# Optimization experiments

Hardware: AMD Instinct MI355X
Metric: run time of the kernel (lower is better)

The kernel has to match this reference:

```python
import jax, jax.numpy as jnp
import numpy as np

B, S, HID = 1, 2048, 2048
NH, NKV, D = 32, 8, 64
GROUPS = NH // NKV
THETA = 10000.0


def _rope_tables(seq_len, dim):
    inv_freq = 1.0 / (THETA ** (jnp.arange(0, dim, 2, dtype=jnp.float32) / dim))
    t = jnp.arange(seq_len, dtype=jnp.float32)
    freqs = jnp.outer(t, inv_freq)            # [S, D/2]
    emb = jnp.concatenate([freqs, freqs], axis=-1)  # [S, D]
    return jnp.cos(emb), jnp.sin(emb)


def _rotate_half(x):
    x1, x2 = jnp.split(x, 2, axis=-1)
    return jnp.concatenate([-x2, x1], axis=-1)


def setup_inputs() -> dict:
    key = jax.random.key(0)
    ks = jax.random.split(key, 8)
    hidden_states = jax.random.normal(ks[0], (B, S, HID), dtype=jnp.float32)
    # additive causal mask, 0 on/below diagonal, -1e9 above
    causal = jnp.tril(jnp.ones((S, S), dtype=bool))
    attention_mask = jnp.where(causal, 0.0, -1e9).astype(jnp.float32)[None, None]
    sc = 0.02
    Wq = sc * jax.random.normal(ks[1], (NH * D, HID), dtype=jnp.float32)
    bq = jnp.zeros((NH * D,), dtype=jnp.float32)
    Wk = sc * jax.random.normal(ks[2], (NKV * D, HID), dtype=jnp.float32)
    bk = jnp.zeros((NKV * D,), dtype=jnp.float32)
    Wv = sc * jax.random.normal(ks[3], (NKV * D, HID), dtype=jnp.float32)
    bv = jnp.zeros((NKV * D,), dtype=jnp.float32)
    Wo = sc * jax.random.normal(ks[4], (HID, NH * D), dtype=jnp.float32)
    return {"hidden_states": hidden_states, "attention_mask": attention_mask,
            "Wq": Wq, "bq": bq, "Wk": Wk, "bk": bk, "Wv": Wv, "bv": bv, "Wo": Wo}


def reference(hidden_states, attention_mask, Wq, bq, Wk, bk, Wv, bv, Wo):
    b, s, _ = hidden_states.shape
    q = (hidden_states @ Wq.T + bq).reshape(b, s, NH, D).transpose(0, 2, 1, 3)   # [B,NH,S,D]
    k = (hidden_states @ Wk.T + bk).reshape(b, s, NKV, D).transpose(0, 2, 1, 3)  # [B,NKV,S,D]
    v = (hidden_states @ Wv.T + bv).reshape(b, s, NKV, D).transpose(0, 2, 1, 3)
    cos, sin = _rope_tables(s, D)
    cos = cos[None, None]; sin = sin[None, None]
    q = q * cos + _rotate_half(q) * sin
    k = k * cos + _rotate_half(k) * sin
    # GQA: repeat KV heads to match query heads
    k = jnp.repeat(k, GROUPS, axis=1)  # [B,NH,S,D]
    v = jnp.repeat(v, GROUPS, axis=1)
    scores = jnp.einsum('bhqd,bhkd->bhqk', q, k) / jnp.sqrt(jnp.float32(D))
    scores = jnp.clip(scores, -50.0, 50.0)
    scores = scores + attention_mask
    probs = jax.nn.softmax(scores.astype(jnp.float32), axis=-1).astype(q.dtype)
    attn = jnp.einsum('bhqk,bhkd->bhqd', probs, v)
    attn = attn.transpose(0, 2, 1, 3).reshape(b, s, NH * D)
    return attn @ Wo.T
```

## Files before the change

kernel.cpp:

```cpp
#include <hip/hip_runtime.h>
#include <hip/hip_bf16.h>
#include <stdint.h>

typedef unsigned short u16;
typedef unsigned int u32;

#define S_LEN 2048
#define HID 2048
#define NH 32
#define NKV 8
#define HD 64
#define PIT 2080

using f32x4 = __attribute__((ext_vector_type(4))) float;
using bfrag = __attribute__((ext_vector_type(8))) short;

__device__ __forceinline__ float b2f(u16 u) {
  union { u32 i; float f; } c; c.i = ((u32)u) << 16; return c.f;
}
__device__ __forceinline__ u16 f2b(float f) {
  union { float f; u32 i; } c; c.f = f;
  u32 r = c.i + 0x7fffu + ((c.i >> 16) & 1u);
  return (u16)(r >> 16);
}
__device__ __forceinline__ uint4 cvt8(const float* __restrict__ p) {
  float4 a = *(const float4*)p;
  float4 b = *(const float4*)(p + 4);
  uint4 r;
  r.x = (u32)f2b(a.x) | ((u32)f2b(a.y) << 16);
  r.y = (u32)f2b(a.z) | ((u32)f2b(a.w) << 16);
  r.z = (u32)f2b(b.x) | ((u32)f2b(b.y) << 16);
  r.w = (u32)f2b(b.z) | ((u32)f2b(b.w) << 16);
  return r;
}

__device__ __forceinline__ void gl2lds16(const u16* g, u16* l) {
  __builtin_amdgcn_global_load_lds(
      (const __attribute__((address_space(1))) void*)g,
      (__attribute__((address_space(3))) void*)l,
      16, 0, 0);
}

#define WAITBAR(N) asm volatile("s_waitcnt vmcnt(" #N ")\ns_barrier" ::: "memory")

__global__ void conv_all(const float* __restrict__ hid, const float* __restrict__ Wq,
                         const float* __restrict__ Wk, const float* __restrict__ Wv,
                         u16* __restrict__ hidb, u16* __restrict__ Wqkvb) {
  int row = blockIdx.x;
  int col = threadIdx.x * 8;
  const float* src; u16* dst;
  if (row < 2048)      { src = hid + (size_t)row * 2048;          dst = hidb  + (size_t)row * PIT; }
  else if (row < 4096) { src = Wq + (size_t)(row - 2048) * 2048;  dst = Wqkvb + (size_t)(row - 2048) * PIT; }
  else if (row < 4608) { src = Wk + (size_t)(row - 4096) * 2048;  dst = Wqkvb + (size_t)(row - 4096 + 2048) * PIT; }
  else                 { src = Wv + (size_t)(row - 4608) * 2048;  dst = Wqkvb + (size_t)(row - 4608 + 2560) * PIT; }
  *(uint4*)(dst + col) = cvt8(src + col);
}

__global__ void conv_all_w(const float* __restrict__ hid, const float* __restrict__ Wq,
                           const float* __restrict__ Wk, const float* __restrict__ Wv,
                           const float* __restrict__ Wo,
                           u16* __restrict__ hidb, u16* __restrict__ Wqkvb,
                           u16* __restrict__ Wob) {
  int row = blockIdx.x;
  int col = threadIdx.x * 8;
  const float* src; u16* dst;
  if (row < 2048)      { src = hid + (size_t)row * 2048;          dst = hidb  + (size_t)row * PIT; }
  else if (row < 4096) { src = Wq + (size_t)(row - 2048) * 2048;  dst = Wqkvb + (size_t)(row - 2048) * PIT; }
  else if (row < 4608) { src = Wk + (size_t)(row - 4096) * 2048;  dst = Wqkvb + (size_t)(row - 4096 + 2048) * PIT; }
  else if (row < 5120) { src = Wv + (size_t)(row - 4608) * 2048;  dst = Wqkvb + (size_t)(row - 4608 + 2560) * PIT; }
  else                 { src = Wo + (size_t)(row - 5120) * 2048;  dst = Wob   + (size_t)(row - 5120) * PIT; }
  *(uint4*)(dst + col) = cvt8(src + col);
}

__global__ void conv_f2b_p(const float* __restrict__ in, u16* __restrict__ out, int n8) {
  int i = blockIdx.x * 256 + threadIdx.x;
  if (i >= n8) return;
  int row = i >> 8;
  int col = (i & 255) * 8;
  *(uint4*)(out + (size_t)row * PIT + col) = cvt8(in + (size_t)row * 2048 + col);
}

__global__ __launch_bounds__(256, 3) void gemm_qkv(
    const u16* __restrict__ A, const u16* __restrict__ B,
    const float* __restrict__ bq, const float* __restrict__ bk, const float* __restrict__ bv,
    u16* __restrict__ Qb, u16* __restrict__ Kb, u16* __restrict__ Vt)
{
  __shared__ __align__(16) u16 As[2 * 4096];
  __shared__ __align__(16) u16 Bs[2 * 8192];

  const int tid  = threadIdx.x;
  const int m0   = blockIdx.y * 64;
  const int n0   = blockIdx.x * 128;
  const int lane = tid & 63;
  const int w    = tid >> 6;
  const int wm   = w >> 1, wn = w & 1;
  const int quad = lane >> 4, l16 = lane & 15;

  const int sr = tid >> 3;
  const int sg = (tid & 7) ^ (sr & 7);
  const u16* gA = A + (size_t)(m0 + sr) * PIT + sg * 8;
  const u16* gB = B + (size_t)(n0 + sr) * PIT + sg * 8;

#define STAGE_G(bi, k0)                                                          \
  do {                                                                           \
    gl2lds16(gA + (k0),                    As + (bi) * 4096 + tid * 8);          \
    gl2lds16(gA + (size_t)32 * PIT + (k0), As + (bi) * 4096 + 2048 + tid * 8);   \
    gl2lds16(gB + (k0),                    Bs + (bi) * 8192 + tid * 8);          \
    gl2lds16(gB + (size_t)32 * PIT + (k0), Bs + (bi) * 8192 + 2048 + tid * 8);   \
    gl2lds16(gB + (size_t)64 * PIT + (k0), Bs + (bi) * 8192 + 4096 + tid * 8);   \
    gl2lds16(gB + (size_t)96 * PIT + (k0), Bs + (bi) * 8192 + 6144 + tid * 8);   \
  } while (0)

  f32x4 zero = {0.f, 0.f, 0.f, 0.f};
  f32x4 acc[2][4];
#pragma unroll
  for (int mi = 0; mi < 2; ++mi)
#pragma unroll
    for (int ni = 0; ni < 4; ++ni) acc[mi][ni] = zero;

  STAGE_G(0, 0);

  int cur = 0;
  for (int k = 0; k < 32; ++k) {
    WAITBAR(0);
    if (k + 1 < 32) STAGE_G(cur ^ 1, (k + 1) * 64);
    const u16* as = As + cur * 4096;
    const u16* bs = Bs + cur * 8192;

#pragma unroll
    for (int kk = 0; kk < 2; ++kk) {
      const int sA = ((kk * 4 + quad) ^ (l16 & 7)) * 8;
      bfrag af[2], bf[4];
#pragma unroll
      for (int i = 0; i < 2; ++i)
        af[i] = *(const bfrag*)&as[(wm * 32 + i * 16 + l16) * 64 + sA];
#pragma unroll
      for (int i = 0; i < 4; ++i)
        bf[i] = *(const bfrag*)&bs[(wn * 64 + i * 16 + l16) * 64 + sA];
#pragma unroll
      for (int mi = 0; mi < 2; ++mi)
#pragma unroll
        for (int ni = 0; ni < 4; ++ni)
          acc[mi][ni] = __builtin_amdgcn_mfma_f32_16x16x32_bf16(af[mi], bf[ni], acc[mi][ni], 0, 0, 0);
    }
    cur ^= 1;
  }
#undef STAGE_G

  __syncthreads();
  u16* strip = As + w * 1152;
  const int rr = lane >> 2;
  const int co = (lane & 3) * 8;

  if (n0 < 2048) {
#pragma unroll
    for (int mi = 0; mi < 2; ++mi) {
#pragma unroll
      for (int n01 = 0; n01 < 2; ++n01)
#pragma unroll
        for (int i = 0; i < 4; ++i) {
          int d  = n01 * 16 + l16;
          int c1 = n0 + wn * 64 + d;
          float x1 = acc[mi][n01][i]     + bq[c1];
          float x2 = acc[mi][n01 + 2][i] + bq[c1 + 32];
          float inv = exp2f(-(float)d * 0.41524101186092034f);
          float ang = (float)(m0 + wm * 32 + mi * 16 + quad * 4 + i) * inv;
          float cs = cosf(ang), sn = sinf(ang);
          strip[(quad * 4 + i) * 72 + d]      = f2b(x1 * cs - x2 * sn);
          strip[(quad * 4 + i) * 72 + d + 32] = f2b(x2 * cs + x1 * sn);
        }
      uint4 v0 = *(const uint4*)&strip[rr * 72 + co];
      uint4 v1 = *(const uint4*)&strip[rr * 72 + 32 + co];
      size_t gb2 = (size_t)(m0 + wm * 32 + mi * 16 + rr) * 2048 + n0 + wn * 64;
      *(uint4*)(Qb + gb2 + co)      = v0;
      *(uint4*)(Qb + gb2 + 32 + co) = v1;
    }
  } else if (n0 < 2560) {
    int cb = (n0 - 2048) + wn * 64;
#pragma unroll
    for (int mi = 0; mi < 2; ++mi) {
#pragma unroll
      for (int n01 = 0; n01 < 2; ++n01)
#pragma unroll
        for (int i = 0; i < 4; ++i) {
          int d  = n01 * 16 + l16;
          int cg = cb + d;
          float x1 = acc[mi][n01][i]     + bk[cg];
          float x2 = acc[mi][n01 + 2][i] + bk[cg + 32];
          float inv = exp2f(-(float)d * 0.41524101186092034f);
          float ang = (float)(m0 + wm * 32 + mi * 16 + quad * 4 + i) * inv;
          float cs = cosf(ang), sn = sinf(ang);
          strip[(quad * 4 + i) * 72 + d]      = f2b(x1 * cs - x2 * sn);
          strip[(quad * 4 + i) * 72 + d + 32] = f2b(x2 * cs + x1 * sn);
        }
      uint4 v0 = *(const uint4*)&strip[rr * 72 + co];
      uint4 v1 = *(const uint4*)&strip[rr * 72 + 32 + co];
      size_t gb2 = (size_t)(m0 + wm * 32 + mi * 16 + rr) * 512 + cb;
      *(uint4*)(Kb + gb2 + co)      = v0;
      *(uint4*)(Kb + gb2 + 32 + co) = v1;
    }
  } else {
    int cgb = (n0 - 2560) + wn * 64;
#pragma unroll
    for (int ni = 0; ni < 4; ++ni) {
      float bvv = bv[cgb + ni * 16 + l16];
#pragma unroll
      for (int mi = 0; mi < 2; ++mi)
#pragma unroll
        for (int i = 0; i < 4; ++i)
          strip[l16 * 72 + mi * 16 + quad * 4 + i] = f2b(acc[mi][ni][i] + bvv);
      uint4 v0 = *(const uint4*)&strip[rr * 72 + co];
      size_t gb2 = (size_t)(cgb + ni * 16 + rr) * PIT + m0 + wm * 32;
      *(uint4*)(Vt + gb2 + co) = v0;
    }
  }
}

__global__ __launch_bounds__(256, 3) void gemm_o(
    const u16* __restrict__ A, const u16* __restrict__ B, float* __restrict__ C)
{
  __shared__ __align__(16) u16 As[2 * 4096];
  __shared__ __align__(16) u16 Bs[2 * 8192];

  const int tid  = threadIdx.x;
  const int m0   = blockIdx.y * 64;
  const int n0   = blockIdx.x * 128;
  const int lane = tid & 63;
  const int w    = tid >> 6;
  const int wm   = w >> 1, wn = w & 1;
  const int quad = lane >> 4, l16 = lane & 15;

  const int sr = tid >> 3;
  const int sg = (tid & 7) ^ (sr & 7);
  const u16* gA = A + (size_t)(m0 + sr) * PIT + sg * 8;
  const u16* gB = B + (size_t)(n0 + sr) * PIT + sg * 8;

#define STAGE_O(bi, k0)                                                          \
  do {                                                                           \
    gl2lds16(gA + (k0),                    As + (bi) * 4096 + tid * 8);          \
    gl2lds16(gA + (size_t)32 * PIT + (k0), As + (bi) * 4096 + 2048 + tid * 8);   \
    gl2lds16(gB + (k0),                    Bs + (bi) * 8192 + tid * 8);          \
    gl2lds16(gB + (size_t)32 * PIT + (k0), Bs + (bi) * 8192 + 2048 + tid * 8);   \
    gl2lds16(gB + (size_t)64 * PIT + (k0), Bs + (bi) * 8192 + 4096 + tid * 8);   \
    gl2lds16(gB + (size_t)96 * PIT + (k0), Bs + (bi) * 8192 + 6144 + tid * 8);   \
  } while (0)

  f32x4 zero = {0.f, 0.f, 0.f, 0.f};
  f32x4 acc[2][4];
#pragma unroll
  for (int mi = 0; mi < 2; ++mi)
#pragma unroll
    for (int ni = 0; ni < 4; ++ni) acc[mi][ni] = zero;

  STAGE_O(0, 0);

  int cur = 0;
  for (int k = 0; k < 32; ++k) {
    WAITBAR(0);
    if (k + 1 < 32) STAGE_O(cur ^ 1, (k + 1) * 64);
    const u16* as = As + cur * 4096;
    const u16* bs = Bs + cur * 8192;

#pragma unroll
    for (int kk = 0; kk < 2; ++kk) {
      const int sA = ((kk * 4 + quad) ^ (l16 & 7)) * 8;
      bfrag af[2], bf[4];
#pragma unroll
      for (int i = 0; i < 2; ++i)
        af[i] = *(const bfrag*)&as[(wm * 32 + i * 16 + l16) * 64 + sA];
#pragma unroll
      for (int i = 0; i < 4; ++i)
        bf[i] = *(const bfrag*)&bs[(wn * 64 + i * 16 + l16) * 64 + sA];
#pragma unroll
      for (int mi = 0; mi < 2; ++mi)
#pragma unroll
        for (int ni = 0; ni < 4; ++ni)
          acc[mi][ni] = __builtin_amdgcn_mfma_f32_16x16x32_bf16(af[mi], bf[ni], acc[mi][ni], 0, 0, 0);
    }
    cur ^= 1;
  }
#undef STAGE_O

#pragma unroll
  for (int ni = 0; ni < 4; ++ni) {
    int col = n0 + wn * 64 + ni * 16 + l16;
#pragma unroll
    for (int mi = 0; mi < 2; ++mi)
#pragma unroll
      for (int i = 0; i < 4; ++i) {
        int row = m0 + wm * 32 + mi * 16 + quad * 4 + i;
        C[(size_t)row * 2048 + col] = acc[mi][ni][i];
      }
  }
}

#define SM_SC 0.18033688011112042f

__global__ __launch_bounds__(256, 2) void attn_flash7(
    const u16* __restrict__ Qb, const u16* __restrict__ Kb,
    const u16* __restrict__ Vt, u16* __restrict__ Ab)
{
  __shared__ __align__(16) u16 Ks[2][2][64 * 64];
  __shared__ __align__(16) u16 Vs[2][2][64 * 64];
  __shared__ __align__(16) u16 Ps[4][16][72];

  const int h    = blockIdx.x;
  const int p    = blockIdx.y;
  const int kvh  = h >> 2;
  const int tid  = threadIdx.x;
  const int lane = tid & 63;
  const int w    = tid >> 6;
  const int quad = lane >> 4, l16 = lane & 15;

  const int qtA = 31 - p, qtB = p;
  const int nA  = qtA + 1;

  const int c0  = w * 128 + lane;
  const int r0  = c0 >> 3,        s0 = c0 & 7;
  const int r1  = (c0 + 64) >> 3, s1 = (c0 + 64) & 7;
  const int sg0 = s0 ^ (r0 & 7);
  const int sg1 = s1 ^ (r1 & 7);
  const u16* Ksrc0 = Kb + (size_t)r0 * 512 + kvh * 64 + sg0 * 8;
  const u16* Ksrc1 = Kb + (size_t)r1 * 512 + kvh * 64 + sg1 * 8;
  const u16* Vsrc0 = Vt + (size_t)(kvh * 64 + r0) * PIT + sg0 * 8;
  const u16* Vsrc1 = Vt + (size_t)(kvh * 64 + r1) * PIT + sg1 * 8;

#define KBOF(t) ((t) < nA ? (t) : (t) - nA)

#define STAGEKV(buf, half, kb)                                                  \
  do {                                                                          \
    gl2lds16(Ksrc0 + (size_t)(kb) * 32768, &Ks[buf][half][0] + c0 * 8);         \
    gl2lds16(Ksrc1 + (size_t)(kb) * 32768, &Ks[buf][half][0] + (c0 + 64) * 8);  \
    gl2lds16(Vsrc0 + (kb) * 64,            &Vs[buf][half][0] + c0 * 8);         \
    gl2lds16(Vsrc1 + (kb) * 64,            &Vs[buf][half][0] + (c0 + 64) * 8);  \
  } while (0)

  STAGEKV(0, 0, 0);
  STAGEKV(0, 1, 1);

  bfrag qfA0, qfA1, qfB0, qfB1;
  {
    const u16* qa = Qb + (size_t)(qtA * 64 + w * 16 + l16) * 2048 + h * 64 + quad * 8;
    const u16* qb = Qb + (size_t)(qtB * 64 + w * 16 + l16) * 2048 + h * 64 + quad * 8;
    qfA0 = *(const bfrag*)qa;  qfA1 = *(const bfrag*)(qa + 32);
    qfB0 = *(const bfrag*)qb;  qfB1 = *(const bfrag*)(qb + 32);
  }
  bfrag q0 = qfA0, q1 = qfA1;

  f32x4 zero = {0.f, 0.f, 0.f, 0.f};
  f32x4 o_acc[4];
  float lpart[4];
#pragma unroll
  for (int nb = 0; nb < 4; ++nb) { o_acc[nb] = zero; lpart[nb] = 0.f; }

  const int swz = (l16 & 7) * 8;
  int qt = qtA;
  int cur = 0;

  for (int T = 0; T < 17; ++T) {
    WAITBAR(0);
    if (T < 16) {
      STAGEKV(cur ^ 1, 0, KBOF(2 * T + 2));
      STAGEKV(cur ^ 1, 1, KBOF(2 * T + 3));
    }

    for (int hh = 0; hh < 2; ++hh) {
      const int t = 2 * T + hh;
      if (t >= 33) break;
      if (t == nA) { q0 = qfB0; q1 = qfB1; qt = qtB; }

      const u16* ks = &Ks[cur][hh][0];
      const u16* vs = &Vs[cur][hh][0];

      bfrag kf0[4], kf1[4];
#pragma unroll
      for (int nb = 0; nb < 4; ++nb) {
        int row = (nb * 16 + l16) * 64;
        kf0[nb] = *(const bfrag*)&ks[row + ((quad * 8) ^ swz)];
        kf1[nb] = *(const bfrag*)&ks[row + ((32 + quad * 8) ^ swz)];
      }

      const bool diag = (t == nA - 1) || (t == 32);

      f32x4 s_acc[4];
      __builtin_amdgcn_s_setprio(1);
#pragma unroll
      for (int nb = 0; nb < 4; ++nb) {
        s_acc[nb] = __builtin_amdgcn_mfma_f32_16x16x32_bf16(q0, kf0[nb], zero, 0, 0, 0);
        s_acc[nb] = __builtin_amdgcn_mfma_f32_16x16x32_bf16(q1, kf1[nb], s_acc[nb], 0, 0, 0);
      }
      __builtin_amdgcn_s_setprio(0);
      if (diag) {
#pragma unroll
        for (int nb = 0; nb < 4; ++nb)
#pragma unroll
          for (int i = 0; i < 4; ++i) {
            float u = s_acc[nb][i] * SM_SC;
            bool msk = (nb * 16 + l16 > w * 16 + quad * 4 + i);
            float pr = msk ? 0.0f : __builtin_amdgcn_exp2f(u);
            lpart[i] += pr;
            Ps[w][quad * 4 + i][nb * 16 + l16] = f2b(pr);
          }
      } else {
#pragma unroll
        for (int nb = 0; nb < 4; ++nb)
#pragma unroll
          for (int i = 0; i < 4; ++i) {
            float u = s_acc[nb][i] * SM_SC;
            float pr = __builtin_amdgcn_exp2f(u);
            lpart[i] += pr;
            Ps[w][quad * 4 + i][nb * 16 + l16] = f2b(pr);
          }
      }

      bfrag vf0[4], vf1[4];
#pragma unroll
      for (int nb = 0; nb < 4; ++nb) {
        int row = (nb * 16 + l16) * 64;
        vf0[nb] = *(const bfrag*)&vs[row + ((quad * 8) ^ swz)];
        vf1[nb] = *(const bfrag*)&vs[row + ((32 + quad * 8) ^ swz)];
      }
      {
        bfrag pf0 = *(const bfrag*)&Ps[w][l16][quad * 8];
        bfrag pf1 = *(const bfrag*)&Ps[w][l16][32 + quad * 8];
        __builtin_amdgcn_s_setprio(1);
#pragma unroll
        for (int nb = 0; nb < 4; ++nb) {
          o_acc[nb] = __builtin_amdgcn_mfma_f32_16x16x32_bf16(pf0, vf0[nb], o_acc[nb], 0, 0, 0);
          o_acc[nb] = __builtin_amdgcn_mfma_f32_16x16x32_bf16(pf1, vf1[nb], o_acc[nb], 0, 0, 0);
        }
        __builtin_amdgcn_s_setprio(0);
      }

      if (diag) {
#pragma unroll
        for (int off = 1; off < 16; off <<= 1)
#pragma unroll
          for (int i = 0; i < 4; ++i)
            lpart[i] += __shfl_xor(lpart[i], off, 64);
#pragma unroll
        for (int i = 0; i < 4; ++i) {
          float inv = 1.0f / lpart[i];
          size_t rbase = (size_t)(qt * 64 + w * 16 + quad * 4 + i) * PIT + h * 64;
#pragma unroll
          for (int nb = 0; nb < 4; ++nb)
            Ab[rbase + nb * 16 + l16] = f2b(o_acc[nb][i] * inv);
        }
#pragma unroll
        for (int nb = 0; nb < 4; ++nb) { o_acc[nb] = zero; lpart[nb] = 0.f; }
      }
    }

    cur ^= 1;
  }
#undef STAGEKV
#undef KBOF
}

extern "C" void kernel_launch(void* const* d_in, const int* in_sizes, int n_in,
                              void* d_out, int out_size, void* d_ws, size_t ws_size,
                              hipStream_t stream) {
  const float* hid = (const float*)d_in[0];
  const float* Wq = (const float*)d_in[2];
  const float* bq = (const float*)d_in[3];
  const float* Wk = (const float*)d_in[4];
  const float* bk = (const float*)d_in[5];
  const float* Wv = (const float*)d_in[6];
  const float* bv = (const float*)d_in[7];
  const float* Wo = (const float*)d_in[8];

  float* Ob = (float*)d_out;

  const size_t need = ((size_t)(2048 + 3072 + 2048 + 512) * PIT + 4194304 + 1048576) * sizeof(u16);

  if (ws_size >= need) {
    u16* hidb  = (u16*)d_ws;
    u16* Wqkvb = hidb + (size_t)2048 * PIT;
    u16* Wob   = Wqkvb + (size_t)3072 * PIT;
    u16* Qb    = Wob + (size_t)2048 * PIT;
    u16* Kb    = Qb + 4194304;
    u16* Vt    = Kb + 1048576;
    u16* Ab    = Wqkvb;

    conv_all_w<<<7168, 256, 0, stream>>>(hid, Wq, Wk, Wv, Wo, hidb, Wqkvb, Wob);
    gemm_qkv<<<dim3(24, 32), 256, 0, stream>>>(hidb, Wqkvb, bq, bk, bv, Qb, Kb, Vt);
    attn_flash7<<<dim3(32, 16), 256, 0, stream>>>(Qb, Kb, Vt, Ab);
    gemm_o<<<dim3(16, 32), 256, 0, stream>>>(Ab, Wob, Ob);
  } else {
    u16* hidb  = (u16*)d_ws;
    u16* Wqkvb = hidb + (size_t)2048 * PIT;
    u16* Qb    = Wqkvb + (size_t)3072 * PIT;
    u16* Kb    = Qb + 4194304;
    u16* Vt    = Kb + 1048576;
    u16* Wob   = hidb;
    u16* Ab    = Wqkvb;

    conv_all<<<5120, 256, 0, stream>>>(hid, Wq, Wk, Wv, hidb, Wqkvb);
    gemm_qkv<<<dim3(24, 32), 256, 0, stream>>>(hidb, Wqkvb, bq, bk, bv, Qb, Kb, Vt);
    conv_f2b_p<<<2048, 256, 0, stream>>>(Wo, Wob, 524288);
    attn_flash7<<<dim3(32, 16), 256, 0, stream>>>(Qb, Kb, Vt, Ab);
    gemm_o<<<dim3(16, 32), 256, 0, stream>>>(Ab, Wob, Ob);
  }
}
```

Before: 228.3 us.

## Share staged K/V tiles between two query heads per attention block

The attention kernel now runs 512-thread blocks covering two query heads of the same KV group, with each set of four waves handling one head. K/V tiles are staged into LDS once per block and used by both heads, halving global-to-LDS traffic per head and the number of loads each thread issues. In exchange the grid is halved to 256 blocks with one block per CU allowed, which lowers block-level parallelism and may leave some CUs idle or less able to hide latency.

Result: no change. 228.8 us (+0.2%).

```diff
diff --git a/kernel.cpp b/kernel.cpp
--- a/kernel.cpp
+++ b/kernel.cpp
@@ -42,19 +42,6 @@
 }
 
 #define WAITBAR(N) asm volatile("s_waitcnt vmcnt(" #N ")\ns_barrier" ::: "memory")
-
-__global__ void conv_all(const float* __restrict__ hid, const float* __restrict__ Wq,
-                         const float* __restrict__ Wk, const float* __restrict__ Wv,
-                         u16* __restrict__ hidb, u16* __restrict__ Wqkvb) {
-  int row = blockIdx.x;
-  int col = threadIdx.x * 8;
-  const float* src; u16* dst;
-  if (row < 2048)      { src = hid + (size_t)row * 2048;          dst = hidb  + (size_t)row * PIT; }
-  else if (row < 4096) { src = Wq + (size_t)(row - 2048) * 2048;  dst = Wqkvb + (size_t)(row - 2048) * PIT; }
-  else if (row < 4608) { src = Wk + (size_t)(row - 4096) * 2048;  dst = Wqkvb + (size_t)(row - 4096 + 2048) * PIT; }
-  else                 { src = Wv + (size_t)(row - 4608) * 2048;  dst = Wqkvb + (size_t)(row - 4608 + 2560) * PIT; }
-  *(uint4*)(dst + col) = cvt8(src + col);
-}
 
 __global__ void conv_all_w(const float* __restrict__ hid, const float* __restrict__ Wq,
                            const float* __restrict__ Wk, const float* __restrict__ Wv,
@@ -72,6 +59,18 @@
   *(uint4*)(dst + col) = cvt8(src + col);
 }
 
+__global__ void conv_all(const float* __restrict__ hid, const float* __restrict__ Wq,
+                         const float* __restrict__ Wk, const float* __restrict__ Wv,
+                         u16* __restrict__ hidb, u16* __restrict__ Wqkvb) {
+  int row = blockIdx.x;
+  int col = threadIdx.x * 8;
+  const float* src; u16* dst;
+  if (row < 2048)      { src = hid + (size_t)row * 2048;          dst = hidb  + (size_t)row * PIT; }
+  else if (row < 4096) { src = Wq + (size_t)(row - 2048) * 2048;  dst = Wqkvb + (size_t)(row - 2048) * PIT; }
+  else if (row < 4608) { src = Wk + (size_t)(row - 4096) * 2048;  dst = Wqkvb + (size_t)(row - 4096 + 2048) * PIT; }
+  else                 { src = Wv + (size_t)(row - 4608) * 2048;  dst = Wqkvb + (size_t)(row - 4608 + 2560) * PIT; }
+  *(uint4*)(dst + col) = cvt8(src + col);
+}
 __global__ void conv_f2b_p(const float* __restrict__ in, u16* __restrict__ out, int n8) {
   int i = blockIdx.x * 256 + threadIdx.x;
   if (i >= n8) return;
@@ -296,43 +295,39 @@
 
 #define SM_SC 0.18033688011112042f
 
-__global__ __launch_bounds__(256, 2) void attn_flash7(
+__global__ __launch_bounds__(512, 1) void attn_flash8(
     const u16* __restrict__ Qb, const u16* __restrict__ Kb,
     const u16* __restrict__ Vt, u16* __restrict__ Ab)
 {
   __shared__ __align__(16) u16 Ks[2][2][64 * 64];
   __shared__ __align__(16) u16 Vs[2][2][64 * 64];
-  __shared__ __align__(16) u16 Ps[4][16][72];
-
-  const int h    = blockIdx.x;
+  __shared__ __align__(16) u16 Ps[8][16][72];
+
+  const int hp   = blockIdx.x;
   const int p    = blockIdx.y;
-  const int kvh  = h >> 2;
+  const int kvh  = hp >> 1;
   const int tid  = threadIdx.x;
   const int lane = tid & 63;
   const int w    = tid >> 6;
+  const int hw   = w >> 2;
+  const int ww   = w & 3;
+  const int h    = hp * 2 + hw;
   const int quad = lane >> 4, l16 = lane & 15;
 
   const int qtA = 31 - p, qtB = p;
   const int nA  = qtA + 1;
 
-  const int c0  = w * 128 + lane;
-  const int r0  = c0 >> 3,        s0 = c0 & 7;
-  const int r1  = (c0 + 64) >> 3, s1 = (c0 + 64) & 7;
-  const int sg0 = s0 ^ (r0 & 7);
-  const int sg1 = s1 ^ (r1 & 7);
-  const u16* Ksrc0 = Kb + (size_t)r0 * 512 + kvh * 64 + sg0 * 8;
-  const u16* Ksrc1 = Kb + (size_t)r1 * 512 + kvh * 64 + sg1 * 8;
-  const u16* Vsrc0 = Vt + (size_t)(kvh * 64 + r0) * PIT + sg0 * 8;
-  const u16* Vsrc1 = Vt + (size_t)(kvh * 64 + r1) * PIT + sg1 * 8;
+  const int r0  = tid >> 3;
+  const int sg0 = (tid & 7) ^ (r0 & 7);
+  const u16* Ksrc = Kb + (size_t)r0 * 512 + kvh * 64 + sg0 * 8;
+  const u16* Vsrc = Vt + (size_t)(kvh * 64 + r0) * PIT + sg0 * 8;
 
 #define KBOF(t) ((t) < nA ? (t) : (t) - nA)
 
 #define STAGEKV(buf, half, kb)                                                  \
   do {                                                                          \
-    gl2lds16(Ksrc0 + (size_t)(kb) * 32768, &Ks[buf][half][0] + c0 * 8);         \
-    gl2lds16(Ksrc1 + (size_t)(kb) * 32768, &Ks[buf][half][0] + (c0 + 64) * 8);  \
-    gl2lds16(Vsrc0 + (kb) * 64,            &Vs[buf][half][0] + c0 * 8);         \
-    gl2lds16(Vsrc1 + (kb) * 64,            &Vs[buf][half][0] + (c0 + 64) * 8);  \
+    gl2lds16(Ksrc + (size_t)(kb) * 32768, &Ks[buf][half][0] + tid * 8);         \
+    gl2lds16(Vsrc + (kb) * 64,            &Vs[buf][half][0] + tid * 8);         \
   } while (0)
 
   STAGEKV(0, 0, 0);
@@ -340,8 +335,8 @@
 
   bfrag qfA0, qfA1, qfB0, qfB1;
   {
-    const u16* qa = Qb + (size_t)(qtA * 64 + w * 16 + l16) * 2048 + h * 64 + quad * 8;
-    const u16* qb = Qb + (size_t)(qtB * 64 + w * 16 + l16) * 2048 + h * 64 + quad * 8;
+    const u16* qa = Qb + (size_t)(qtA * 64 + ww * 16 + l16) * 2048 + h * 64 + quad * 8;
+    const u16* qb = Qb + (size_t)(qtB * 64 + ww * 16 + l16) * 2048 + h * 64 + quad * 8;
     qfA0 = *(const bfrag*)qa;  qfA1 = *(const bfrag*)(qa + 32);
     qfB0 = *(const bfrag*)qb;  qfB1 = *(const bfrag*)(qb + 32);
   }
@@ -396,7 +391,7 @@
 #pragma unroll
           for (int i = 0; i < 4; ++i) {
             float u = s_acc[nb][i] * SM_SC;
-            bool msk = (nb * 16 + l16 > w * 16 + quad * 4 + i);
+            bool msk = (nb * 16 + l16 > ww * 16 + quad * 4 + i);
             float pr = msk ? 0.0f : __builtin_amdgcn_exp2f(u);
             lpart[i] += pr;
             Ps[w][quad * 4 + i][nb * 16 + l16] = f2b(pr);
@@ -441,7 +436,7 @@
 #pragma unroll
         for (int i = 0; i < 4; ++i) {
           float inv = 1.0f / lpart[i];
-          size_t rbase = (size_t)(qt * 64 + w * 16 + quad * 4 + i) * PIT + h * 64;
+          size_t rbase = (size_t)(qt * 64 + ww * 16 + quad * 4 + i) * PIT + h * 64;
 #pragma unroll
           for (int nb = 0; nb < 4; ++nb)
             Ab[rbase + nb * 16 + l16] = f2b(o_acc[nb][i] * inv);
@@ -484,7 +479,7 @@
 
     conv_all_w<<<7168, 256, 0, stream>>>(hid, Wq, Wk, Wv, Wo, hidb, Wqkvb, Wob);
     gemm_qkv<<<dim3(24, 32), 256, 0, stream>>>(hidb, Wqkvb, bq, bk, bv, Qb, Kb, Vt);
-    attn_flash7<<<dim3(32, 16), 256, 0, stream>>>(Qb, Kb, Vt, Ab);
+    attn_flash8<<<dim3(16, 16), 512, 0, stream>>>(Qb, Kb, Vt, Ab);
     gemm_o<<<dim3(16, 32), 256, 0, stream>>>(Ab, Wob, Ob);
   } else {
     u16* hidb  = (u16*)d_ws;
@@ -498,7 +493,7 @@
     conv_all<<<5120, 256, 0, stream>>>(hid, Wq, Wk, Wv, hidb, Wqkvb);
     gemm_qkv<<<dim3(24, 32), 256, 0, stream>>>(hidb, Wqkvb, bq, bk, bv, Qb, Kb, Vt);
     conv_f2b_p<<<2048, 256, 0, stream>>>(Wo, Wob, 524288);
-    attn_flash7<<<dim3(32, 16), 256, 0, stream>>>(Qb, Kb, Vt, Ab);
+    attn_flash8<<<dim3(16, 16), 512, 0, stream>>>(Qb, Kb, Vt, Ab);
     gemm_o<<<dim3(16, 32), 256, 0, stream>>>(Ab, Wob, Ob);
   }
 }
```
